# Optimization experiments

Measured on AMD Instinct MI355X. Metric: run time of the kernel, lower is better.

The kernel has to match this reference:

```python
import jax, jax.numpy as jnp
import numpy as np

HEADS = 8
DK = 64            # key_size == size_per_head
NEIGHBORS = 3
KSIZE = 1 + 2 * NEIGHBORS  # 7 (rate=1)


def setup_inputs() -> dict:
    key = jax.random.key(0)
    k1, k2, k3, k4 = jax.random.split(key, 4)
    B, HW, S, D = 2, 64, 256, 512
    inputs = jax.random.normal(k1, (B, HW, S, D), dtype=jnp.float32)
    pos_bias = jax.random.normal(k2, (HEADS, S, KSIZE), dtype=jnp.float32)
    W_qkv = jax.random.normal(k3, (D, 3 * HEADS * DK), dtype=jnp.float32) * 0.02
    W_out = jax.random.normal(k4, (HEADS * DK, D), dtype=jnp.float32) * 0.02
    return {"inputs": inputs, "pos_bias": pos_bias, "W_qkv": W_qkv, "W_out": W_out}


def reference(inputs, pos_bias, W_qkv, W_out):
    B, HW, S, D = inputs.shape
    # qkv projection (no bias), split into q, k, v
    qkv = inputs @ W_qkv                                   # [B,HW,S,3*H*DK]
    q, k, v = jnp.split(qkv, 3, axis=-1)
    q = (q / jnp.sqrt(jnp.float32(DK))).reshape(B, HW, S, HEADS, DK)
    k = k.reshape(B, HW, S, HEADS, DK)
    v = v.reshape(B, HW, S, HEADS, DK)

    # zero-pad keys/values along seq (faithful to F.pad with value=0)
    pad = NEIGHBORS
    kp = jnp.pad(k, ((0, 0), (0, 0), (pad, pad), (0, 0), (0, 0)))
    vp = jnp.pad(v, ((0, 0), (0, 0), (pad, pad), (0, 0), (0, 0)))

    # sliding-window gather: window w for query i covers padded positions i..i+KSIZE-1
    idx = jnp.arange(S)[:, None] + jnp.arange(KSIZE)[None, :]  # [S,KSIZE]
    kw = kp[:, :, idx]                                         # [B,HW,S,KSIZE,H,DK]
    vw = vp[:, :, idx]                                         # [B,HW,S,KSIZE,H,DK]

    # scores over the window
    attn = jnp.einsum('bnshd,bnswhd->bnswh', q, kw)            # [B,HW,S,KSIZE,H]
    # additive positional bias: [H,S,KSIZE] -> [S,KSIZE,H] broadcast
    attn = attn + jnp.transpose(pos_bias, (1, 2, 0))[None, None]
    attn = jax.nn.softmax(attn, axis=-2)                       # softmax over window dim

    out = jnp.einsum('bnswh,bnswhd->bnshd', attn, vw)          # [B,HW,S,H,DK]
    out = out.reshape(B, HW, S, HEADS * DK)
    return out @ W_out
```

## Files before the change

kernel.cpp:

```cpp
#include <hip/hip_runtime.h>
#include <hip/hip_bf16.h>
#include <cstdint>


typedef __bf16 bf16x8 __attribute__((ext_vector_type(8)));
typedef float f32x4 __attribute__((ext_vector_type(4)));

__device__ __forceinline__ uint16_t f2bf(float f) {
    uint32_t u = __builtin_bit_cast(uint32_t, f);
    return (uint16_t)((u + 0x7fffu + ((u >> 16) & 1u)) >> 16);
}
__device__ __forceinline__ float bflo(uint32_t u) { return __builtin_bit_cast(float, u << 16); }
__device__ __forceinline__ float bfhi(uint32_t u) { return __builtin_bit_cast(float, u & 0xffff0000u); }

__device__ __forceinline__ void unpack8(uint4 v, float* f) {
    f[0] = bflo(v.x); f[1] = bfhi(v.x);
    f[2] = bflo(v.y); f[3] = bfhi(v.y);
    f[4] = bflo(v.z); f[5] = bfhi(v.z);
    f[6] = bflo(v.w); f[7] = bfhi(v.w);
}
__device__ __forceinline__ uint32_t pack2(float a, float b) {
    return (uint32_t)f2bf(a) | ((uint32_t)f2bf(b) << 16);
}

#define GLOAD_LDS16(gp, lp)                                                        \
    __builtin_amdgcn_global_load_lds((const __attribute__((address_space(1))) void*)(gp), \
                                     (__attribute__((address_space(3))) void*)(lp), 16, 0, 0)

__device__ __forceinline__ bf16x8 ds_read16(const uint16_t* p) {
    bf16x8 r;
    asm volatile("ds_read_b128 %0, %1"
                 : "=v"(r)
                 : "v"((const __attribute__((address_space(3))) void*)p));
    return r;
}

__global__ void prep(const float* __restrict__ X, const float* __restrict__ Wqkv,
                     const float* __restrict__ Wout, uint16_t* __restrict__ Xb,
                     uint16_t* __restrict__ WqkvT, uint16_t* __restrict__ WoutT) {
    int b = blockIdx.x;
    if (b < 8192) {
        int i = b * 256 + threadIdx.x;
        const float4* p = (const float4*)X + (size_t)i * 2;
        float4 a = p[0], q = p[1];
        uint4 o;
        o.x = pack2(a.x, a.y);
        o.y = pack2(a.z, a.w);
        o.z = pack2(q.x, q.y);
        o.w = pack2(q.z, q.w);
        *((uint4*)Xb + i) = o;
    } else {
        int idx = (b - 8192) * 256 + threadIdx.x;
        if (idx < 512 * 1536) {
            int r = idx / 1536, c = idx - r * 1536;
            WqkvT[(size_t)c * 512 + r] = f2bf(Wqkv[idx]);
        } else {
            idx -= 512 * 1536;
            int r = idx >> 9, c = idx & 511;
            WoutT[(size_t)c * 512 + r] = f2bf(Wout[idx]);
        }
    }
}

__global__ __launch_bounds__(512, 2)
void gemm_qkv_attn(const uint16_t* __restrict__ Xb, const uint16_t* __restrict__ WqkvT,
                   const float* __restrict__ pb, uint16_t* __restrict__ attn) {
    __shared__ __align__(16) uint16_t lds[54016];

    constexpr int KO = 16384;
    constexpr int VO = 33152;
    constexpr int PO = 49920;

    const int tid  = threadIdx.x;
    const int lane = tid & 63;
    const int wv   = tid >> 6;
    const int r    = lane & 15;
    const int quad = lane >> 4;
    const int wr   = wv >> 1;
    const int wc   = wv & 1;
    const int h    = blockIdx.x >> 7;
    const int bn   = blockIdx.x & 127;
    const long bm0 = (long)bn * 256;
    const int NT   = 16;

#define SRC_ROWCOL(d_, row_, col_) do {                                                 \
        int ln_ = (d_) >> 3, pre_ = ((d_) & 7) ^ (ln_ & 7);                             \
        row_ = 2 * ln_ + (pre_ >> 2);                                                   \
        col_ = (pre_ & 3) * 8;                                                          \
    } while (0)
    int rA0, cA0, rA1, cA1, rB0, cB0, rB1, cB1;
    SRC_ROWCOL(tid,        rA0, cA0);
    SRC_ROWCOL(tid + 512,  rA1, cA1);
    SRC_ROWCOL(tid,        rB0, cB0);
    SRC_ROWCOL(tid + 512,  rB1, cB1);
#undef SRC_ROWCOL
    const long gB0 = ((long)(rB0 >> 6)) * 512 + h * 64 + (rB0 & 63);
    const long gB1 = ((long)(rB1 >> 6)) * 512 + h * 64 + (rB1 & 63);
    const uint16_t* pA0 = Xb + (bm0 + rA0) * 512L + cA0;
    const uint16_t* pA1 = Xb + (bm0 + rA1) * 512L + cA1;
    const uint16_t* pB0 = WqkvT + gB0 * 512 + cB0;
    const uint16_t* pB1 = WqkvT + gB1 * 512 + cB1;

#define STAGE(b_, t_) do {                                                              \
        GLOAD_LDS16(pA0 + (t_) * 32, &lds[(b_) * 8192 + tid * 8]);                      \
        GLOAD_LDS16(pA1 + (t_) * 32, &lds[(b_) * 8192 + (tid + 512) * 8]);              \
        GLOAD_LDS16(pB0 + (t_) * 32, &lds[16384 + (b_) * 6144 + tid * 8]);              \
        if (tid < 256)                                                                  \
            GLOAD_LDS16(pB1 + (t_) * 32, &lds[16384 + (b_) * 6144 + (tid + 512) * 8]);  \
    } while (0)

    const int p_ln  = (((r & 1) << 2) | quad) ^ ((r >> 1) & 7);
    const int aLane = wr * 2048 + (r >> 1) * 64 + p_ln * 8;
    const int bLane = 16384 + wc * 3072 + (r >> 1) * 64 + p_ln * 8;

#define DS_A(mf_) ds_read16(&lds[aoff + aLane + (mf_) * 512])
#define DS_B(nf_) ds_read16(&lds[boff + bLane + (nf_) * 512])
#define WAITK(n_) do { asm volatile("s_waitcnt lgkmcnt(" #n_ ")" ::: "memory");         \
                       __builtin_amdgcn_sched_barrier(0); } while (0)

    f32x4 acc[4][6];
#pragma unroll
    for (int mf = 0; mf < 4; ++mf)
#pragma unroll
        for (int nf = 0; nf < 6; ++nf) acc[mf][nf] = (f32x4){0.f, 0.f, 0.f, 0.f};

    STAGE(0, 0);
    asm volatile("s_waitcnt vmcnt(0)" ::: "memory");
    __builtin_amdgcn_s_barrier();

    for (int t = 0; t < NT; ++t) {
        const int b    = t & 1;
        const int aoff = b * 8192;
        const int boff = b * 6144;
        const bool pf  = (t + 1 < NT);

        if (pf) STAGE(b ^ 1, t + 1);

        bf16x8 bfr[6], a0, a1, a2, a3;
#pragma unroll
        for (int nf = 0; nf < 6; ++nf) bfr[nf] = DS_B(nf);
        a0 = DS_A(0); a1 = DS_A(1);
        a2 = DS_A(2); a3 = DS_A(3);

        WAITK(2);
        __builtin_amdgcn_s_setprio(1);
#pragma unroll
        for (int nf = 0; nf < 6; ++nf) {
            acc[0][nf] = __builtin_amdgcn_mfma_f32_16x16x32_bf16(bfr[nf], a0, acc[0][nf], 0, 0, 0);
            acc[1][nf] = __builtin_amdgcn_mfma_f32_16x16x32_bf16(bfr[nf], a1, acc[1][nf], 0, 0, 0);
        }
        __builtin_amdgcn_s_setprio(0);

        WAITK(0);
        __builtin_amdgcn_s_setprio(1);
#pragma unroll
        for (int nf = 0; nf < 6; ++nf) {
            acc[2][nf] = __builtin_amdgcn_mfma_f32_16x16x32_bf16(bfr[nf], a2, acc[2][nf], 0, 0, 0);
            acc[3][nf] = __builtin_amdgcn_mfma_f32_16x16x32_bf16(bfr[nf], a3, acc[3][nf], 0, 0, 0);
        }
        __builtin_amdgcn_s_setprio(0);

        if (pf) {
            asm volatile("s_waitcnt vmcnt(0)" ::: "memory");
            __builtin_amdgcn_s_barrier();
        }
    }

    asm volatile("s_waitcnt vmcnt(0) lgkmcnt(0)" ::: "memory");
    __builtin_amdgcn_s_barrier();

    if (tid < 96) {
        int a    = tid / 48;
        int rem  = tid - a * 48;
        int hr6  = rem >> 3;
        int c8   = rem & 7;
        int hrow = (hr6 < 3) ? hr6 : (256 + hr6);
        ((uint4*)&lds[a ? VO : KO])[hrow * 8 + c8] = (uint4){0u, 0u, 0u, 0u};
    }

#pragma unroll
    for (int nf = 0; nf < 6; ++nf) {
        int arr, d0;
        if (wc == 0) { if (nf < 4) { arr = 0; d0 = nf * 16; } else { arr = 1; d0 = (nf - 4) * 16; } }
        else         { if (nf < 2) { arr = 1; d0 = 32 + nf * 16; } else { arr = 2; d0 = (nf - 2) * 16; } }
        const int base = (arr == 0) ? 0 : ((arr == 1) ? KO : VO);
        const int hofs = (arr == 0) ? 0 : 3;
        const int cc0  = (d0 >> 3) + (quad >> 1);
        const int sub  = (quad & 1) * 4;
#pragma unroll
        for (int mf = 0; mf < 4; ++mf) {
            int rowX = wr * 64 + mf * 16 + r + hofs;
            uint2 w;
            w.x = pack2(acc[mf][nf][0], acc[mf][nf][1]);
            w.y = pack2(acc[mf][nf][2], acc[mf][nf][3]);
            *(uint2*)&lds[base + rowX * 64 + ((cc0 ^ (rowX & 7)) << 3) + sub] = w;
        }
    }
    __syncthreads();

    const int s     = tid & 255;
    const int half  = tid >> 8;
    const int cbase = half * 4;
    float* pp = (float*)&lds[PO];

    uint4 qc[4];
    const uint4* qarr = (const uint4*)lds;
#pragma unroll
    for (int c = 0; c < 4; ++c) qc[c] = qarr[s * 8 + ((cbase + c) ^ (s & 7))];

    float sc[7];
#pragma unroll
    for (int w = 0; w < 7; ++w) sc[w] = 0.f;
    const uint4* karr = (const uint4*)&lds[KO];
#pragma unroll
    for (int c = 0; c < 4; ++c) {
        float qf[8];
        unpack8(qc[c], qf);
#pragma unroll
        for (int w = 0; w < 7; ++w) {
            int hrow = s + w;
            uint4 kc = karr[hrow * 8 + ((cbase + c) ^ (hrow & 7))];
            float kf[8];
            unpack8(kc, kf);
#pragma unroll
            for (int j = 0; j < 8; ++j) sc[w] += qf[j] * kf[j];
        }
    }

    if (half == 1) {
#pragma unroll
        for (int w = 0; w < 7; ++w) pp[s * 8 + w] = sc[w];
    }
    __syncthreads();

    if (half == 0) {
        const float* pbr = pb + ((size_t)h * 256 + s) * 7;
        float mx = -1e30f, tot[7];
#pragma unroll
        for (int w = 0; w < 7; ++w) {
            tot[w] = (sc[w] + pp[s * 8 + w]) * 0.125f + pbr[w];
            mx = fmaxf(mx, tot[w]);
        }
        float sum = 0.f;
#pragma unroll
        for (int w = 0; w < 7; ++w) {
            tot[w] = __expf(tot[w] - mx);
            sum += tot[w];
        }
        const float inv = 1.f / sum;
#pragma unroll
        for (int w = 0; w < 7; ++w) pp[s * 8 + w] = tot[w] * inv;
    }
    __syncthreads();

    float p[7];
#pragma unroll
    for (int w = 0; w < 7; ++w) p[w] = pp[s * 8 + w];

    const uint4* varr = (const uint4*)&lds[VO];
    uint4 ov[4];
#pragma unroll
    for (int c = 0; c < 4; ++c) {
        float o[8] = {0.f, 0.f, 0.f, 0.f, 0.f, 0.f, 0.f, 0.f};
#pragma unroll
        for (int w = 0; w < 7; ++w) {
            int hrow = s + w;
            uint4 vc = varr[hrow * 8 + ((cbase + c) ^ (hrow & 7))];
            float vf[8];
            unpack8(vc, vf);
#pragma unroll
            for (int j = 0; j < 8; ++j) o[j] += p[w] * vf[j];
        }
        ov[c].x = pack2(o[0], o[1]);
        ov[c].y = pack2(o[2], o[3]);
        ov[c].z = pack2(o[4], o[5]);
        ov[c].w = pack2(o[6], o[7]);
    }
    uint16_t* orow = attn + ((size_t)(bn * 256 + s)) * 512 + h * 64 + cbase * 8;
#pragma unroll
    for (int c = 0; c < 4; ++c) *(uint4*)(orow + c * 8) = ov[c];
#undef STAGE
#undef DS_A
#undef DS_B
#undef WAITK
}

template <bool F32OUT>
__global__ __launch_bounds__(512, 4)
void gemm_mn(const uint16_t* __restrict__ A, const uint16_t* __restrict__ BT,
             void* __restrict__ Cout, int M, int N, int K) {
    __shared__ __align__(16) uint16_t lds[36864];

    const int tid  = threadIdx.x;
    const int lane = tid & 63;
    const int wv   = tid >> 6;
    const int r    = lane & 15;
    const int quad = lane >> 4;
    const int wr   = wv >> 1;
    const int wc   = wv & 1;
    const long bm0 = (long)blockIdx.x * 256;
    const long bn0 = (long)blockIdx.y * 128;
    const int NT   = K >> 5;

#define SRC_ROWCOL(d_, row_, col_) do {                                                 \
        int ln_ = (d_) >> 3, pre_ = ((d_) & 7) ^ (ln_ & 7);                             \
        row_ = 2 * ln_ + (pre_ >> 2);                                                   \
        col_ = (pre_ & 3) * 8;                                                          \
    } while (0)
    int rA0, cA0, rA1, cA1, rB0, cB0;
    SRC_ROWCOL(tid,       rA0, cA0);
    SRC_ROWCOL(tid + 512, rA1, cA1);
    SRC_ROWCOL(tid,       rB0, cB0);
    const uint16_t* pA0 = A  + (bm0 + rA0) * (long)K + cA0;
    const uint16_t* pA1 = A  + (bm0 + rA1) * (long)K + cA1;
    const uint16_t* pB0 = BT + (bn0 + rB0) * (long)K + cB0;
#undef SRC_ROWCOL

#define STAGE(b_, t_) do {                                                              \
        GLOAD_LDS16(pA0 + (t_) * 32, &lds[(b_) * 8192 + tid * 8]);                      \
        GLOAD_LDS16(pA1 + (t_) * 32, &lds[(b_) * 8192 + (tid + 512) * 8]);              \
        GLOAD_LDS16(pB0 + (t_) * 32, &lds[24576 + (b_) * 4096 + tid * 8]);              \
    } while (0)

    const int p_ln  = (((r & 1) << 2) | quad) ^ ((r >> 1) & 7);
    const int aLane = wr * 2048 + (r >> 1) * 64 + p_ln * 8;
    const int bLane = 24576 + wc * 2048 + (r >> 1) * 64 + p_ln * 8;

#define DS_A(mf_) ds_read16(&lds[aoff + aLane + (mf_) * 512])
#define DS_B(nf_) ds_read16(&lds[boff + bLane + (nf_) * 512])
#define WAITK2 do { asm volatile("s_waitcnt lgkmcnt(2)" ::: "memory");                  \
                    __builtin_amdgcn_sched_barrier(0); } while (0)
#define WAITK0 do { asm volatile("s_waitcnt lgkmcnt(0)" ::: "memory");                  \
                    __builtin_amdgcn_sched_barrier(0); } while (0)
#define MFMA_CL(m0_, f0_, f1_)                                                          \
    __builtin_amdgcn_s_setprio(1);                                                      \
    _Pragma("unroll")                                                                   \
    for (int nf = 0; nf < 4; ++nf)                                                      \
        acc[(m0_)][nf] = __builtin_amdgcn_mfma_f32_16x16x32_bf16(bfr[nf], f0_,          \
                                                                 acc[(m0_)][nf], 0, 0, 0); \
    _Pragma("unroll")                                                                   \
    for (int nf = 0; nf < 4; ++nf)                                                      \
        acc[(m0_) + 1][nf] = __builtin_amdgcn_mfma_f32_16x16x32_bf16(bfr[nf], f1_,      \
                                                                 acc[(m0_) + 1][nf], 0, 0, 0); \
    __builtin_amdgcn_s_setprio(0);

    f32x4 acc[4][4];
#pragma unroll
    for (int mf = 0; mf < 4; ++mf)
#pragma unroll
        for (int nf = 0; nf < 4; ++nf) acc[mf][nf] = (f32x4){0.f, 0.f, 0.f, 0.f};

    STAGE(0, 0);
    STAGE(1, 1);
    asm volatile("s_waitcnt vmcnt(3)" ::: "memory");
    __builtin_amdgcn_s_barrier();

    int b = 0, bs = 2;
    for (int t = 0; t < NT; ++t) {
        const int aoff = b * 8192;
        const int boff = b * 4096;

        if (t + 2 < NT) STAGE(bs, t + 2);

        bf16x8 bfr[4], a0, a1, a2, a3;
#pragma unroll
        for (int nf = 0; nf < 4; ++nf) bfr[nf] = DS_B(nf);
        a0 = DS_A(0); a1 = DS_A(1);
        a2 = DS_A(2); a3 = DS_A(3);

        WAITK2;
        MFMA_CL(0, a0, a1)
        WAITK0;
        MFMA_CL(2, a2, a3)

        if (t + 1 < NT) {
            if (t + 2 < NT)
                asm volatile("s_waitcnt vmcnt(3)" ::: "memory");
            else
                asm volatile("s_waitcnt vmcnt(0)" ::: "memory");
            __builtin_amdgcn_s_barrier();
        }
        b  = (b  == 2) ? 0 : b + 1;
        bs = (bs == 2) ? 0 : bs + 1;
    }

#pragma unroll
    for (int mf = 0; mf < 4; ++mf) {
        long m = bm0 + wr * 64 + mf * 16 + r;
#pragma unroll
        for (int nf = 0; nf < 4; ++nf) {
            long n0 = bn0 + wc * 64 + nf * 16 + quad * 4;
            if (F32OUT) {
                float4 v = {acc[mf][nf][0], acc[mf][nf][1], acc[mf][nf][2], acc[mf][nf][3]};
                *(float4*)((float*)Cout + m * (long)N + n0) = v;
            } else {
                uint2 w;
                w.x = pack2(acc[mf][nf][0], acc[mf][nf][1]);
                w.y = pack2(acc[mf][nf][2], acc[mf][nf][3]);
                *(uint2*)((uint16_t*)Cout + m * (long)N + n0) = w;
            }
        }
    }
#undef STAGE
#undef DS_A
#undef DS_B
#undef WAITK2
#undef WAITK0
#undef MFMA_CL
}

extern "C" void kernel_launch(void* const* d_in, const int* in_sizes, int n_in,
                              void* d_out, int out_size, void* d_ws, size_t ws_size,
                              hipStream_t stream) {
    const float* X    = (const float*)d_in[0];
    const float* pb   = (const float*)d_in[1];
    const float* Wqkv = (const float*)d_in[2];
    const float* Wout = (const float*)d_in[3];
    float* out = (float*)d_out;

    char* ws = (char*)d_ws;
    uint16_t* WqkvT = (uint16_t*)(ws);
    uint16_t* WoutT = (uint16_t*)(ws + 1572864);
    uint16_t* Xb    = (uint16_t*)(ws + 2097152);
    uint16_t* attnb = (uint16_t*)(ws + 35651584);

    prep<<<12288, 256, 0, stream>>>(X, Wqkv, Wout, Xb, WqkvT, WoutT);
    gemm_qkv_attn<<<1024, 512, 0, stream>>>(Xb, WqkvT, pb, attnb);
    gemm_mn<true><<<dim3(128, 4), 512, 0, stream>>>(attnb, WoutT, out, 32768, 512, 512);
}
```

Measured before the change: 228.5 us.

## Deepen QKV GEMM pipeline to 4-stage LDS ring with register double-buffering

Replaces the two-buffer LDS prefetch in the fused QKV+attention kernel with a four-slot ring that keeps up to three tiles of global loads in flight. It also prefetches the next tile's LDS fragments into a second register set while the current tile's MFMAs run. Global loads now go to specialised waves: waves 0-3 load A, waves 4-6 load B and wave 7 loads nothing. The aim is to hide global and LDS latency behind MFMA work. In exchange it uses more LDS (57344 vs 54016 halves, about 112 KiB vs about 105 KiB) and more VGPRs, which could pressure the 2-blocks-per-CU occupancy target.

```diff
diff --git a/kernel.cpp b/kernel.cpp
--- a/kernel.cpp
+++ b/kernel.cpp
@@ -65,7 +65,7 @@
 __global__ __launch_bounds__(512, 2)
 void gemm_qkv_attn(const uint16_t* __restrict__ Xb, const uint16_t* __restrict__ WqkvT,
                    const float* __restrict__ pb, uint16_t* __restrict__ attn) {
-    __shared__ __align__(16) uint16_t lds[54016];
+    __shared__ __align__(16) uint16_t lds[57344];
 
     constexpr int KO = 16384;
     constexpr int VO = 33152;
@@ -81,42 +81,41 @@
     const int h    = blockIdx.x >> 7;
     const int bn   = blockIdx.x & 127;
     const long bm0 = (long)bn * 256;
-    const int NT   = 16;
-
-#define SRC_ROWCOL(d_, row_, col_) do {                                                 \
-        int ln_ = (d_) >> 3, pre_ = ((d_) & 7) ^ (ln_ & 7);                             \
-        row_ = 2 * ln_ + (pre_ >> 2);                                                   \
-        col_ = (pre_ & 3) * 8;                                                          \
-    } while (0)
-    int rA0, cA0, rA1, cA1, rB0, cB0, rB1, cB1;
-    SRC_ROWCOL(tid,        rA0, cA0);
-    SRC_ROWCOL(tid + 512,  rA1, cA1);
-    SRC_ROWCOL(tid,        rB0, cB0);
-    SRC_ROWCOL(tid + 512,  rB1, cB1);
-#undef SRC_ROWCOL
-    const long gB0 = ((long)(rB0 >> 6)) * 512 + h * 64 + (rB0 & 63);
-    const long gB1 = ((long)(rB1 >> 6)) * 512 + h * 64 + (rB1 & 63);
-    const uint16_t* pA0 = Xb + (bm0 + rA0) * 512L + cA0;
-    const uint16_t* pA1 = Xb + (bm0 + rA1) * 512L + cA1;
-    const uint16_t* pB0 = WqkvT + gB0 * 512 + cB0;
-    const uint16_t* pB1 = WqkvT + gB1 * 512 + cB1;
-
-#define STAGE(b_, t_) do {                                                              \
-        GLOAD_LDS16(pA0 + (t_) * 32, &lds[(b_) * 8192 + tid * 8]);                      \
-        GLOAD_LDS16(pA1 + (t_) * 32, &lds[(b_) * 8192 + (tid + 512) * 8]);              \
-        GLOAD_LDS16(pB0 + (t_) * 32, &lds[16384 + (b_) * 6144 + tid * 8]);              \
-        if (tid < 256)                                                                  \
-            GLOAD_LDS16(pB1 + (t_) * 32, &lds[16384 + (b_) * 6144 + (tid + 512) * 8]);  \
+
+    const uint16_t* srcp[4];
+    int rel[4];
+#pragma unroll
+    for (int i = 0; i < 4; ++i) {
+        int j = wv * 256 + i * 64 + lane;
+        if (j < 1024) {
+            int d = j, ln = d >> 3, pre = (d & 7) ^ (ln & 7);
+            int row = 2 * ln + (pre >> 2), col = (pre & 3) * 8;
+            srcp[i] = Xb + (bm0 + row) * 512L + col;
+            rel[i]  = d * 8;
+        } else {
+            int e = j - 1024, ln = e >> 3, pre = (e & 7) ^ (ln & 7);
+            int row = 2 * ln + (pre >> 2), col = (pre & 3) * 8;
+            long grow = ((long)(row >> 6)) * 512 + h * 64 + (row & 63);
+            srcp[i] = WqkvT + grow * 512 + col;
+            rel[i]  = e * 8;
+        }
+    }
+
+#define STAGE(q_, t_) do {                                                              \
+        if (wv < 4) {                                                                   \
+            _Pragma("unroll")                                                           \
+            for (int i_ = 0; i_ < 4; ++i_)                                              \
+                GLOAD_LDS16(srcp[i_] + (t_) * 32, &lds[(q_) * 8192 + rel[i_]]);         \
+        } else if (wv < 7) {                                                            \
+            _Pragma("unroll")                                                           \
+            for (int i_ = 0; i_ < 4; ++i_)                                              \
+                GLOAD_LDS16(srcp[i_] + (t_) * 32, &lds[32768 + (q_) * 6144 + rel[i_]]); \
+        }                                                                               \
     } while (0)
 
     const int p_ln  = (((r & 1) << 2) | quad) ^ ((r >> 1) & 7);
     const int aLane = wr * 2048 + (r >> 1) * 64 + p_ln * 8;
-    const int bLane = 16384 + wc * 3072 + (r >> 1) * 64 + p_ln * 8;
-
-#define DS_A(mf_) ds_read16(&lds[aoff + aLane + (mf_) * 512])
-#define DS_B(nf_) ds_read16(&lds[boff + bLane + (nf_) * 512])
-#define WAITK(n_) do { asm volatile("s_waitcnt lgkmcnt(" #n_ ")" ::: "memory");         \
-                       __builtin_amdgcn_sched_barrier(0); } while (0)
+    const int bLane = wc * 3072 + (r >> 1) * 64 + p_ln * 8;
 
     f32x4 acc[4][6];
 #pragma unroll
@@ -124,46 +123,51 @@
 #pragma unroll
         for (int nf = 0; nf < 6; ++nf) acc[mf][nf] = (f32x4){0.f, 0.f, 0.f, 0.f};
 
+    bf16x8 fA0[4], fB0[6], fA1[4], fB1[6];
+
+#define READS(q_, FA_, FB_) do {                                                        \
+        const int ao_ = (q_) * 8192, bo_ = 32768 + (q_) * 6144;                         \
+        _Pragma("unroll")                                                               \
+        for (int nf_ = 0; nf_ < 6; ++nf_) FB_[nf_] = ds_read16(&lds[bo_ + bLane + nf_ * 512]); \
+        _Pragma("unroll")                                                               \
+        for (int mf_ = 0; mf_ < 4; ++mf_) FA_[mf_] = ds_read16(&lds[ao_ + aLane + mf_ * 512]); \
+    } while (0)
+
+#define BODY(t_, FAn_, FBn_, FAc_, FBc_) do {                                           \
+        if ((t_) + 1 < 16) {                                                            \
+            READS(((t_) + 1) & 3, FAn_, FBn_);                                          \
+            asm volatile("s_waitcnt lgkmcnt(10)" ::: "memory");                         \
+        } else {                                                                        \
+            asm volatile("s_waitcnt lgkmcnt(0)" ::: "memory");                          \
+        }                                                                               \
+        __builtin_amdgcn_sched_barrier(0);                                              \
+        __builtin_amdgcn_s_setprio(1);                                                  \
+        _Pragma("unroll")                                                               \
+        for (int nf_ = 0; nf_ < 6; ++nf_)                                               \
+            _Pragma("unroll")                                                           \
+            for (int mf_ = 0; mf_ < 4; ++mf_)                                           \
+                acc[mf_][nf_] = __builtin_amdgcn_mfma_f32_16x16x32_bf16(                \
+                    FBc_[nf_], FAc_[mf_], acc[mf_][nf_], 0, 0, 0);                      \
+        __builtin_amdgcn_s_setprio(0);                                                  \
+        if ((t_) + 3 < 16) {                                                            \
+            STAGE(((t_) + 3) & 3, (t_) + 3);                                            \
+            asm volatile("s_waitcnt vmcnt(4)" ::: "memory");                            \
+        } else {                                                                        \
+            asm volatile("s_waitcnt vmcnt(0)" ::: "memory");                            \
+        }                                                                               \
+        if ((t_) < 15) __builtin_amdgcn_s_barrier();                                    \
+    } while (0)
+
     STAGE(0, 0);
-    asm volatile("s_waitcnt vmcnt(0)" ::: "memory");
+    STAGE(1, 1);
+    STAGE(2, 2);
+    asm volatile("s_waitcnt vmcnt(4)" ::: "memory");
     __builtin_amdgcn_s_barrier();
-
-    for (int t = 0; t < NT; ++t) {
-        const int b    = t & 1;
-        const int aoff = b * 8192;
-        const int boff = b * 6144;
-        const bool pf  = (t + 1 < NT);
-
-        if (pf) STAGE(b ^ 1, t + 1);
-
-        bf16x8 bfr[6], a0, a1, a2, a3;
-#pragma unroll
-        for (int nf = 0; nf < 6; ++nf) bfr[nf] = DS_B(nf);
-        a0 = DS_A(0); a1 = DS_A(1);
-        a2 = DS_A(2); a3 = DS_A(3);
-
-        WAITK(2);
-        __builtin_amdgcn_s_setprio(1);
-#pragma unroll
-        for (int nf = 0; nf < 6; ++nf) {
-            acc[0][nf] = __builtin_amdgcn_mfma_f32_16x16x32_bf16(bfr[nf], a0, acc[0][nf], 0, 0, 0);
-            acc[1][nf] = __builtin_amdgcn_mfma_f32_16x16x32_bf16(bfr[nf], a1, acc[1][nf], 0, 0, 0);
-        }
-        __builtin_amdgcn_s_setprio(0);
-
-        WAITK(0);
-        __builtin_amdgcn_s_setprio(1);
-#pragma unroll
-        for (int nf = 0; nf < 6; ++nf) {
-            acc[2][nf] = __builtin_amdgcn_mfma_f32_16x16x32_bf16(bfr[nf], a2, acc[2][nf], 0, 0, 0);
-            acc[3][nf] = __builtin_amdgcn_mfma_f32_16x16x32_bf16(bfr[nf], a3, acc[3][nf], 0, 0, 0);
-        }
-        __builtin_amdgcn_s_setprio(0);
-
-        if (pf) {
-            asm volatile("s_waitcnt vmcnt(0)" ::: "memory");
-            __builtin_amdgcn_s_barrier();
-        }
+    READS(0, fA0, fB0);
+
+    for (int tt = 0; tt < 16; tt += 2) {
+        BODY(tt,     fA1, fB1, fA0, fB0);
+        BODY(tt + 1, fA0, fB0, fA1, fB1);
     }
 
     asm volatile("s_waitcnt vmcnt(0) lgkmcnt(0)" ::: "memory");
@@ -280,9 +284,8 @@
 #pragma unroll
     for (int c = 0; c < 4; ++c) *(uint4*)(orow + c * 8) = ov[c];
 #undef STAGE
-#undef DS_A
-#undef DS_B
-#undef WAITK
+#undef READS
+#undef BODY
 }
 
 template <bool F32OUT>
```

Result: no change. 230.7 us (+0.9%).
